# Performance work log

Hardware: AMD Instinct MI355X
Metric: run time of the kernel (lower is better)

Reference implementation:

```python
import jax, jax.numpy as jnp
import numpy as np

B, T, F, U = 128, 512, 512, 256

def hard_sigmoid(x):
    # Keras K.hard_sigmoid
    return jnp.clip(0.2 * x + 0.5, 0.0, 1.0)

def setup_inputs() -> dict:
    key = jax.random.key(0)
    ks = jax.random.split(key, 10)
    def glorot(k, shp):
        fan_in, fan_out = shp[0], shp[-1]
        std = np.sqrt(2.0 / (fan_in + fan_out)).astype(np.float32)
        return jax.random.normal(k, shp, jnp.float32) * std
    return {
        "x": jax.random.normal(ks[0], (B, T, F), jnp.float32),
        "kernel": glorot(ks[1], (F, 4 * U)),
        "recurrent_kernel": glorot(ks[2], (U, 4 * U)),
        "attention_h": glorot(ks[3], (F + U, U)),
        "attention_c": glorot(ks[4], (F + U, U)),
        "attention1": glorot(ks[5], (2 * U + F, U)),
        "biase1": glorot(ks[6], (U,)),
        "attention2": glorot(ks[7], (U, 1)),
        "attention2_2": glorot(ks[8], (U, 1)),
        "biase2": glorot(ks[9], (U,)),
    }

def _run_direction(x_tbf, xg_tbg, rk, Wh, Wc, units):
    # x_tbf: (T,B,F); xg_tbg: (T,B,4U) precomputed x @ kernel (same math as per-step dot)
    Bn = x_tbf.shape[1]
    z = jnp.zeros((Bn, units), x_tbf.dtype)
    carry0 = (z, z, z, z, z, z, z, z)

    def att_weights(states, Ws, xt):
        # softmax over L2 norms of tanh(concat(state, x) @ W) for 4 history states
        scores = []
        for s, W in zip(states, Ws):
            a = jnp.tanh(jnp.concatenate([s, xt], axis=1) @ W)  # (B,U)
            scores.append(jnp.sqrt(jnp.sum(a * a, axis=1)))     # (B,)
        return jax.nn.softmax(jnp.stack(scores, axis=1), axis=1)  # (B,4)

    def step(carry, inp):
        xt, xg = inp
        h1, c1, h2, c2, h3, c3, h4, c4 = carry
        wh = att_weights([h1, h2, h3, h4], [Wh, Wh, Wh, Wh], xt)
        hmix = jax.nn.relu(wh[:, 0:1] * h1 + wh[:, 1:2] * h2 + wh[:, 2:3] * h3 + wh[:, 3:4] * h4)
        # NOTE: original code (faithfully kept) uses attention_h for the 4th cell-state score
        wc = att_weights([c1, c2, c3, c4], [Wc, Wc, Wc, Wh], xt)
        cmix = jax.nn.relu(wc[:, 0:1] * c1 + wc[:, 1:2] * c2 + wc[:, 2:3] * c3 + wc[:, 3:4] * c4)
        g = xg + hmix @ rk  # (B,4U), gate order [i, f, c, o]
        i = hard_sigmoid(g[:, :units])
        f = hard_sigmoid(g[:, units:2 * units])
        m = hard_sigmoid(g[:, 2 * units:3 * units])  # candidate uses hard_sigmoid in original
        o = hard_sigmoid(g[:, 3 * units:])
        c = f * cmix + i * m
        h = o * jnp.tanh(c)
        # history shift: [h, c, h_tm1, c_tm1, h_tm2, c_tm2, h_tm3, c_tm3]
        return (h, c, h1, c1, h2, c2, h3, c3), h

    _, hs = jax.lax.scan(step, carry0, (x_tbf, xg_tbg))
    return hs  # (T,B,U)

def reference(x, kernel, recurrent_kernel, attention_h, attention_c,
              attention1, biase1, attention2, attention2_2, biase2):
    units = recurrent_kernel.shape[0]
    x_tbf = jnp.transpose(x, (1, 0, 2))              # (T,B,F)
    xg = jnp.einsum('tbf,fg->tbg', x_tbf, kernel)    # (T,B,4U)
    fwd = _run_direction(x_tbf, xg, recurrent_kernel, attention_h, attention_c, units)
    bwd = _run_direction(x_tbf[::-1], xg[::-1], recurrent_kernel, attention_h, attention_c, units)[::-1]
    outs = jnp.concatenate([fwd, bwd], axis=-1)      # (T,B,2U)
    outs = jnp.transpose(outs, (1, 0, 2))            # (B,T,2U)
    # intra attention (vectorized over time, equivalent to the per-step loop + reshape)
    A11 = attention1[:2 * units, :]
    A12 = attention1[2 * units:, :]
    ha = jax.nn.relu(outs @ A11 + 0.0 * biase1) @ attention2        # (B,T,1)
    hb = jax.nn.relu(x @ A12 + 0.0 * biase2) @ attention2_2         # (B,T,1)
    return jnp.tanh(ha * outs + hb)                                  # (B,T,2U)
```

## Files before the change

### kernel.cpp

```cpp
#include <hip/hip_runtime.h>
#include <cstddef>
#include <cstdint>

#define DEVINL __device__ __forceinline__

constexpr int Bn = 128;
constexpr int Tn = 512;
constexpr int Fn = 512;
constexpr int Un = 256;
constexpr int Gn = 1024;
constexpr int RS = 5;

typedef _Float16 h2t   __attribute__((ext_vector_type(2)));
typedef _Float16 half4 __attribute__((ext_vector_type(4)));
typedef _Float16 half8 __attribute__((ext_vector_type(8)));
typedef float    f32x4 __attribute__((ext_vector_type(4)));

DEVINL float ftanh(float x) { float e = __expf(2.f * x); return 1.f - 2.f / (e + 1.f); }
DEVINL float hsig(float x)  { return fminf(fmaxf(fmaf(x, 0.2f, 0.5f), 0.f), 1.f); }

DEVINL void softmax4(float* s) {
    float mx = fmaxf(fmaxf(s[0], s[1]), fmaxf(s[2], s[3]));
    float e0 = __expf(s[0] - mx), e1 = __expf(s[1] - mx);
    float e2 = __expf(s[2] - mx), e3 = __expf(s[3] - mx);
    float inv = 1.f / (e0 + e1 + e2 + e3);
    s[0] = e0 * inv; s[1] = e1 * inv; s[2] = e2 * inv; s[3] = e3 * inv;
}

DEVINL float d2(unsigned int w, unsigned int h, float acc) {
#if __has_builtin(__builtin_amdgcn_fdot2)
    return __builtin_amdgcn_fdot2(__builtin_bit_cast(h2t, w), __builtin_bit_cast(h2t, h), acc, false);
#else
    h2t a = __builtin_bit_cast(h2t, w), b = __builtin_bit_cast(h2t, h);
    acc = fmaf((float)a.x, (float)b.x, acc);
    acc = fmaf((float)a.y, (float)b.y, acc);
    return acc;
#endif
}
DEVINL float dot8h(uint4 w, uint4 h, float acc) {
    acc = d2(w.x, h.x, acc);
    acc = d2(w.y, h.y, acc);
    acc = d2(w.z, h.z, acc);
    acc = d2(w.w, h.w, acc);
    return acc;
}

__global__ __launch_bounds__(256)
void pack_x(const float* __restrict__ x, _Float16* __restrict__ xh)
{
    size_t i = ((size_t)blockIdx.x * 256 + threadIdx.x) * 4;
    float4 v = *(const float4*)(x + i);
    half4 o;
    o.x = (_Float16)v.x; o.y = (_Float16)v.y; o.z = (_Float16)v.z; o.w = (_Float16)v.w;
    *(half4*)(xh + i) = o;
}

__global__ __launch_bounds__(256)
void wt_pack(const float* __restrict__ W, _Float16* __restrict__ Wt, int N)
{
    int total = N * 512;
    for (int e = blockIdx.x * 256 + threadIdx.x; e < total; e += gridDim.x * 256) {
        int n = e >> 9, k = e & 511;
        Wt[e] = (_Float16)W[(size_t)k * N + n];
    }
}

__global__ __launch_bounds__(256)
void pack_w(const float* __restrict__ rk, const float* __restrict__ ath,
            const float* __restrict__ atc,
            _Float16* __restrict__ rkP, _Float16* __restrict__ WhP,
            _Float16* __restrict__ WcP)
{
    int idx = blockIdx.x * 256 + threadIdx.x;
    const int stride = gridDim.x * 256;
    for (int e = idx; e < 32 * 1024 * 8; e += stride) {
        int i = e & 7, n = (e >> 3) & 1023, kc = e >> 13;
        rkP[e] = (_Float16)rk[(size_t)(kc * 8 + i) * Gn + n];
    }
    for (int e = idx; e < 32 * 256 * 8; e += stride) {
        int i = e & 7, n = (e >> 3) & 255, kc = e >> 11;
        WhP[e] = (_Float16)ath[(size_t)(kc * 8 + i) * Un + n];
        WcP[e] = (_Float16)atc[(size_t)(kc * 8 + i) * Un + n];
    }
}

template<bool TMAJ>
__global__ __launch_bounds__(256)
void gemm_mfma(const _Float16* __restrict__ A, const _Float16* __restrict__ Wt,
               int N, _Float16* __restrict__ out)
{
    __shared__ __align__(16) _Float16 As[64][40];
    __shared__ __align__(16) _Float16 Bs[64][40];
    const int tid = threadIdx.x;
    const int n0 = blockIdx.x * 64, m0 = blockIdx.y * 64;
    const int w = tid >> 6, lane = tid & 63;
    const int fr = lane & 15, quad = lane >> 4;
    const int srow = tid >> 2, sk = (tid & 3) * 8;

    f32x4 acc[4];
    #pragma unroll
    for (int i = 0; i < 4; i++) acc[i] = (f32x4){0.f, 0.f, 0.f, 0.f};

    const _Float16* ap = A  + (size_t)(m0 + srow) * 512 + sk;
    const _Float16* bp = Wt + (size_t)(n0 + srow) * 512 + sk;

    for (int k0 = 0; k0 < 512; k0 += 32) {
        uint4 av = *(const uint4*)(ap + k0);
        uint4 bv = *(const uint4*)(bp + k0);
        __syncthreads();
        *(uint4*)&As[srow][sk] = av;
        *(uint4*)&Bs[srow][sk] = bv;
        __syncthreads();
        half8 a = *(const half8*)&As[w * 16 + fr][quad * 8];
        #pragma unroll
        for (int nt = 0; nt < 4; nt++) {
            half8 b = *(const half8*)&Bs[nt * 16 + fr][quad * 8];
            acc[nt] = __builtin_amdgcn_mfma_f32_16x16x32_f16(a, b, acc[nt], 0, 0, 0);
        }
    }
    #pragma unroll
    for (int nt = 0; nt < 4; nt++) {
        int n = n0 + nt * 16 + fr;
        #pragma unroll
        for (int reg = 0; reg < 4; reg++) {
            int m = m0 + w * 16 + quad * 4 + reg;
            if (TMAJ) {
                int b = m >> 9, t = m & 511;
                out[((size_t)t * Bn + b) * N + n] = (_Float16)acc[nt][reg];
            } else {
                out[(size_t)m * N + n] = (_Float16)acc[nt][reg];
            }
        }
    }
}

__global__ __launch_bounds__(512)
void recurrence(const _Float16* __restrict__ xg,
                const _Float16* __restrict__ xWh,
                const _Float16* __restrict__ xWc,
                const _Float16* __restrict__ rkP,
                const _Float16* __restrict__ WhP,
                const _Float16* __restrict__ WcP,
                _Float16* __restrict__ outs)
{
    const int tid = threadIdx.x;
    const int d = blockIdx.x >> 6;
    const int b0 = (blockIdx.x & 63) * 2;

    __shared__ float Hr[2][RS][Un], Cr[2][RS][Un];
    __shared__ float PHr[2][RS][Un], PCcr[2][RS][Un], PChr[2][RS][Un];
    __shared__ __align__(16) unsigned int hm_pk[2][128];
    __shared__ __align__(16) unsigned int Hpk[2][128], Cpk[2][128];
    __shared__ float gtmp[2][4][Un];
    __shared__ float red[2][8][4];
    __shared__ float wsm[2][8];

    for (int e = tid; e < 2 * RS * Un; e += 512) {
        ((float*)Hr)[e] = 0.f; ((float*)Cr)[e] = 0.f;
        ((float*)PHr)[e] = 0.f; ((float*)PCcr)[e] = 0.f; ((float*)PChr)[e] = 0.f;
    }
    __syncthreads();

    const int r = tid >> 8, u = tid & 255;
    const int lane = tid & 63, wv = tid >> 6;

    for (int t = 0; t < Tn; t++) {
        const int tt = d ? (Tn - 1 - t) : t;
        const int st = t % RS;
        int sj[4];
        #pragma unroll
        for (int j = 0; j < 4; j++) sj[j] = (t - 1 - j + 2 * RS) % RS;

        const size_t rowx = (size_t)tt * Bn + (b0 + r);

        float xh  = (float)xWh[rowx * Un + u];
        float xc  = (float)xWc[rowx * Un + u];
        float xg0 = (float)xg[rowx * Gn + u];
        float xg1 = (float)xg[rowx * Gn + Un + u];
        float xg2 = (float)xg[rowx * Gn + 2 * Un + u];
        float xg3 = (float)xg[rowx * Gn + 3 * Un + u];

        float vals[8];
        #pragma unroll
        for (int j = 0; j < 4; j++) {
            float ah = ftanh(PHr[r][sj[j]][u] + xh);
            vals[j] = ah * ah;
            float pc  = (j < 3) ? PCcr[r][sj[j]][u] : PChr[r][sj[j]][u];
            float ac = ftanh(pc + ((j < 3) ? xc : xh));
            vals[4 + j] = ac * ac;
        }
        #pragma unroll
        for (int jj = 0; jj < 8; jj++) {
            float v = vals[jj];
            #pragma unroll
            for (int m = 32; m; m >>= 1) v += __shfl_xor(v, m, 64);
            if (lane == 0) red[r][jj][wv & 3] = v;
        }
        __syncthreads();
        if (tid < 4) {
            int rr = tid >> 1, hf = tid & 1;
            float s[4];
            #pragma unroll
            for (int j = 0; j < 4; j++) {
                const float* q = red[rr][hf * 4 + j];
                s[j] = sqrtf(q[0] + q[1] + q[2] + q[3]);
            }
            softmax4(s);
            #pragma unroll
            for (int j = 0; j < 4; j++) wsm[rr][hf * 4 + j] = s[j];
        }
        __syncthreads();

        float ha = 0.f, ca = 0.f;
        #pragma unroll
        for (int j = 0; j < 4; j++) {
            ha = fmaf(wsm[r][j],     Hr[r][sj[j]][u], ha);
            ca = fmaf(wsm[r][4 + j], Cr[r][sj[j]][u], ca);
        }
        float hmv = fmaxf(ha, 0.f);
        float cmv = fmaxf(ca, 0.f);
        {
            float ho = __shfl_xor(hmv, 1, 64);
            if (!(tid & 1)) {
                h2t pk; pk.x = (_Float16)hmv; pk.y = (_Float16)ho;
                hm_pk[r][u >> 1] = __builtin_bit_cast(unsigned int, pk);
            }
        }
        __syncthreads();

        float a00 = 0.f, a01 = 0.f, a10 = 0.f, a11 = 0.f;
        {
            const _Float16* p1 = rkP + (size_t)tid * 8;
            const _Float16* p2 = rkP + (size_t)(tid + 512) * 8;
            #pragma unroll 4
            for (int kc = 0; kc < 32; kc++) {
                uint4 w1 = *(const uint4*)(p1 + (size_t)kc * 8192);
                uint4 w2 = *(const uint4*)(p2 + (size_t)kc * 8192);
                uint4 h0 = *(const uint4*)&hm_pk[0][kc * 4];
                uint4 h1 = *(const uint4*)&hm_pk[1][kc * 4];
                a00 = dot8h(w1, h0, a00); a01 = dot8h(w2, h0, a01);
                a10 = dot8h(w1, h1, a10); a11 = dot8h(w2, h1, a11);
            }
        }
        {
            int q1 = tid >> 8, u1 = tid & 255;
            gtmp[0][q1][u1] = a00;  gtmp[0][q1 + 2][u1] = a01;
            gtmp[1][q1][u1] = a10;  gtmp[1][q1 + 2][u1] = a11;
        }
        __syncthreads();

        {
            float g0 = gtmp[r][0][u] + xg0;
            float g1 = gtmp[r][1][u] + xg1;
            float g2 = gtmp[r][2][u] + xg2;
            float g3 = gtmp[r][3][u] + xg3;
            float gi = hsig(g0), gf = hsig(g1), gm = hsig(g2), go = hsig(g3);
            float c = gf * cmv + gi * gm;
            float h = go * ftanh(c);
            Hr[r][st][u] = h;
            Cr[r][st][u] = c;
            outs[(((size_t)(b0 + r)) * Tn + tt) * 512 + d * 256 + u] = (_Float16)h;
            float hho = __shfl_xor(h, 1, 64);
            float cco = __shfl_xor(c, 1, 64);
            if (!(tid & 1)) {
                h2t pk1; pk1.x = (_Float16)h; pk1.y = (_Float16)hho;
                h2t pk2; pk2.x = (_Float16)c; pk2.y = (_Float16)cco;
                Hpk[r][u >> 1] = __builtin_bit_cast(unsigned int, pk1);
                Cpk[r][u >> 1] = __builtin_bit_cast(unsigned int, pk2);
            }
        }
        __syncthreads();

        if (tid < 256) {
            const int c = tid;
            const _Float16* pw = WhP + (size_t)c * 8;
            float ph0 = 0.f, ph1 = 0.f, pc0 = 0.f, pc1 = 0.f;
            #pragma unroll 4
            for (int kc = 0; kc < 32; kc++) {
                uint4 wv4 = *(const uint4*)(pw + (size_t)kc * 2048);
                uint4 H0 = *(const uint4*)&Hpk[0][kc * 4];
                uint4 H1 = *(const uint4*)&Hpk[1][kc * 4];
                uint4 C0 = *(const uint4*)&Cpk[0][kc * 4];
                uint4 C1 = *(const uint4*)&Cpk[1][kc * 4];
                ph0 = dot8h(wv4, H0, ph0); ph1 = dot8h(wv4, H1, ph1);
                pc0 = dot8h(wv4, C0, pc0); pc1 = dot8h(wv4, C1, pc1);
            }
            PHr[0][st][c] = ph0; PHr[1][st][c] = ph1;
            PChr[0][st][c] = pc0; PChr[1][st][c] = pc1;
        } else {
            const int c = tid - 256;
            const _Float16* pw = WcP + (size_t)c * 8;
            float pc0 = 0.f, pc1 = 0.f;
            #pragma unroll 4
            for (int kc = 0; kc < 32; kc++) {
                uint4 wv4 = *(const uint4*)(pw + (size_t)kc * 2048);
                uint4 C0 = *(const uint4*)&Cpk[0][kc * 4];
                uint4 C1 = *(const uint4*)&Cpk[1][kc * 4];
                pc0 = dot8h(wv4, C0, pc0); pc1 = dot8h(wv4, C1, pc1);
            }
            PCcr[0][st][c] = pc0; PCcr[1][st][c] = pc1;
        }
        __syncthreads();
    }
}

DEVINL void cvt8(uint4 v, float* f) {
    h2t p0 = __builtin_bit_cast(h2t, v.x), p1 = __builtin_bit_cast(h2t, v.y);
    h2t p2 = __builtin_bit_cast(h2t, v.z), p3 = __builtin_bit_cast(h2t, v.w);
    f[0] = (float)p0.x; f[1] = (float)p0.y; f[2] = (float)p1.x; f[3] = (float)p1.y;
    f[4] = (float)p2.x; f[5] = (float)p2.y; f[6] = (float)p3.x; f[7] = (float)p3.y;
}

__global__ __launch_bounds__(256)
void final2(const _Float16* __restrict__ t1, const _Float16* __restrict__ t2,
            const _Float16* __restrict__ outs16,
            const float* __restrict__ at2, const float* __restrict__ at22,
            float* __restrict__ out)
{
    __shared__ float has[8], hbs[8];
    const int tid = threadIdx.x;
    const size_t m0 = (size_t)blockIdx.x * 8;
    const int rr = tid >> 5, us = tid & 31;
    const size_t m = m0 + rr;

    uint4 v1 = *(const uint4*)(t1 + m * 256 + us * 8);
    uint4 v2 = *(const uint4*)(t2 + m * 256 + us * 8);
    float f1[8], f2[8];
    cvt8(v1, f1); cvt8(v2, f2);
    float4 wa0 = *(const float4*)(at2  + us * 8);
    float4 wa1 = *(const float4*)(at2  + us * 8 + 4);
    float4 wb0 = *(const float4*)(at22 + us * 8);
    float4 wb1 = *(const float4*)(at22 + us * 8 + 4);

    float pa = fmaxf(f1[0], 0.f) * wa0.x + fmaxf(f1[1], 0.f) * wa0.y
             + fmaxf(f1[2], 0.f) * wa0.z + fmaxf(f1[3], 0.f) * wa0.w
             + fmaxf(f1[4], 0.f) * wa1.x + fmaxf(f1[5], 0.f) * wa1.y
             + fmaxf(f1[6], 0.f) * wa1.z + fmaxf(f1[7], 0.f) * wa1.w;
    float pb = fmaxf(f2[0], 0.f) * wb0.x + fmaxf(f2[1], 0.f) * wb0.y
             + fmaxf(f2[2], 0.f) * wb0.z + fmaxf(f2[3], 0.f) * wb0.w
             + fmaxf(f2[4], 0.f) * wb1.x + fmaxf(f2[5], 0.f) * wb1.y
             + fmaxf(f2[6], 0.f) * wb1.z + fmaxf(f2[7], 0.f) * wb1.w;
    #pragma unroll
    for (int mm = 16; mm; mm >>= 1) {
        pa += __shfl_xor(pa, mm, 32);
        pb += __shfl_xor(pb, mm, 32);
    }
    if (us == 0) { has[rr] = pa; hbs[rr] = pb; }
    __syncthreads();

    for (int e = tid; e < 8 * 128; e += 256) {
        int r2 = e >> 7, k4 = (e & 127) * 4;
        size_t base = (m0 + r2) * 512 + k4;
        uint2 hv = *(const uint2*)(outs16 + base);
        h2t pA = __builtin_bit_cast(h2t, hv.x), pB = __builtin_bit_cast(h2t, hv.y);
        float hav = has[r2], hbv = hbs[r2];
        float4 o;
        o.x = ftanh(hav * (float)pA.x + hbv);
        o.y = ftanh(hav * (float)pA.y + hbv);
        o.z = ftanh(hav * (float)pB.x + hbv);
        o.w = ftanh(hav * (float)pB.y + hbv);
        *(float4*)(out + base) = o;
    }
}

extern "C" void kernel_launch(void* const* d_in, const int* in_sizes, int n_in,
                              void* d_out, int out_size, void* d_ws, size_t ws_size,
                              hipStream_t stream)
{
    (void)in_sizes; (void)n_in; (void)out_size; (void)ws_size;
    const float* x    = (const float*)d_in[0];
    const float* wk   = (const float*)d_in[1];
    const float* rk   = (const float*)d_in[2];
    const float* ath  = (const float*)d_in[3];
    const float* atc  = (const float*)d_in[4];
    const float* at1  = (const float*)d_in[5];
    const float* at2  = (const float*)d_in[7];
    const float* at22 = (const float*)d_in[8];
    float* out = (float*)d_out;

    char* p = (char*)d_ws;
    auto take = [&](size_t bytes) { char* q = p; p += (bytes + 255) & ~(size_t)255; return q; };
    _Float16* xg   = (_Float16*)take((size_t)Tn * Bn * Gn * 2);
    _Float16* xWh  = (_Float16*)take((size_t)Tn * Bn * Un * 2);
    _Float16* xWc  = (_Float16*)take((size_t)Tn * Bn * Un * 2);
    _Float16* A16  = (_Float16*)take((size_t)Bn * Tn * 512 * 2);
    _Float16* xf16 = (_Float16*)take((size_t)Bn * Tn * Fn * 2);
    _Float16* rkP  = (_Float16*)take((size_t)Un * Gn * 2);
    _Float16* WhP  = (_Float16*)take((size_t)Un * Un * 2);
    _Float16* WcP  = (_Float16*)take((size_t)Un * Un * 2);
    _Float16* Wt1  = (_Float16*)take((size_t)Gn * Fn * 2);
    _Float16* Wt2  = (_Float16*)take((size_t)Un * Fn * 2);
    _Float16* Wt3  = (_Float16*)take((size_t)Un * Fn * 2);
    _Float16* WtA  = (_Float16*)take((size_t)Un * Fn * 2);
    _Float16* WtB  = (_Float16*)take((size_t)Un * Fn * 2);
    _Float16* t1 = (_Float16*)xg;
    _Float16* t2 = t1 + (size_t)Bn * Tn * Un;

    pack_x<<<32768, 256, 0, stream>>>(x, xf16);
    wt_pack<<<2048, 256, 0, stream>>>(wk, Wt1, Gn);
    wt_pack<<<1024, 256, 0, stream>>>(ath + (size_t)Un * Un, Wt2, Un);
    wt_pack<<<1024, 256, 0, stream>>>(atc + (size_t)Un * Un, Wt3, Un);
    wt_pack<<<1024, 256, 0, stream>>>(at1, WtA, Un);
    wt_pack<<<1024, 256, 0, stream>>>(at1 + (size_t)512 * Un, WtB, Un);
    pack_w<<<64, 256, 0, stream>>>(rk, ath, atc, rkP, WhP, WcP);

    gemm_mfma<true><<<dim3(Gn / 64, (Bn * Tn) / 64), 256, 0, stream>>>(xf16, Wt1, Gn, xg);
    gemm_mfma<true><<<dim3(Un / 64, (Bn * Tn) / 64), 256, 0, stream>>>(xf16, Wt2, Un, xWh);
    gemm_mfma<true><<<dim3(Un / 64, (Bn * Tn) / 64), 256, 0, stream>>>(xf16, Wt3, Un, xWc);

    recurrence<<<dim3(128), dim3(512), 0, stream>>>(xg, xWh, xWc, rkP, WhP, WcP, A16);

    gemm_mfma<false><<<dim3(Un / 64, (Bn * Tn) / 64), 256, 0, stream>>>(A16,  WtA, Un, t1);
    gemm_mfma<false><<<dim3(Un / 64, (Bn * Tn) / 64), 256, 0, stream>>>(xf16, WtB, Un, t2);
    final2<<<(Bn * Tn) / 8, 256, 0, stream>>>(t1, t2, A16, at2, at22, out);
}
```

Baseline: 5.469 ms.

## Double recurrence block to 1024 threads and fold softmax into all threads

```diff
diff --git a/kernel.cpp b/kernel.cpp
--- a/kernel.cpp
+++ b/kernel.cpp
@@ -134,7 +134,7 @@
     }
 }
 
-__global__ __launch_bounds__(512)
+__global__ __launch_bounds__(1024)
 void recurrence(const _Float16* __restrict__ xg,
                 const _Float16* __restrict__ xWh,
                 const _Float16* __restrict__ xWc,
@@ -152,17 +152,20 @@
     __shared__ __align__(16) unsigned int hm_pk[2][128];
     __shared__ __align__(16) unsigned int Hpk[2][128], Cpk[2][128];
     __shared__ float gtmp[2][4][Un];
-    __shared__ float red[2][8][4];
-    __shared__ float wsm[2][8];
-
-    for (int e = tid; e < 2 * RS * Un; e += 512) {
+    __shared__ __align__(16) float red[2][8][4];
+
+    for (int e = tid; e < 2 * RS * Un; e += 1024) {
         ((float*)Hr)[e] = 0.f; ((float*)Cr)[e] = 0.f;
         ((float*)PHr)[e] = 0.f; ((float*)PCcr)[e] = 0.f; ((float*)PChr)[e] = 0.f;
     }
     __syncthreads();
 
-    const int r = tid >> 8, u = tid & 255;
-    const int lane = tid & 63, wv = tid >> 6;
+    const int r2  = tid >> 9;
+    const int g   = (tid >> 8) & 1;
+    const int u   = tid & 255;
+    const int lane = tid & 63;
+    const int gwv = (tid >> 6) & 3;
+    const int r   = (tid >> 8) & 1;
 
     for (int t = 0; t < Tn; t++) {
         const int tt = d ? (Tn - 1 - t) : t;
@@ -171,55 +174,61 @@
         #pragma unroll
         for (int j = 0; j < 4; j++) sj[j] = (t - 1 - j + 2 * RS) % RS;
 
-        const size_t rowx = (size_t)tt * Bn + (b0 + r);
-
-        float xh  = (float)xWh[rowx * Un + u];
-        float xc  = (float)xWc[rowx * Un + u];
-        float xg0 = (float)xg[rowx * Gn + u];
-        float xg1 = (float)xg[rowx * Gn + Un + u];
-        float xg2 = (float)xg[rowx * Gn + 2 * Un + u];
-        float xg3 = (float)xg[rowx * Gn + 3 * Un + u];
-
-        float vals[8];
+        const size_t rowS = (size_t)tt * Bn + (b0 + r2);
+        float xh = (float)xWh[rowS * Un + u];
+        float xc = (float)xWc[rowS * Un + u];
+        float xg0 = 0.f, xg1 = 0.f, xg2 = 0.f, xg3 = 0.f;
+        if (tid < 512) {
+            const size_t rowG = (size_t)tt * Bn + (b0 + r);
+            xg0 = (float)xg[rowG * Gn + u];
+            xg1 = (float)xg[rowG * Gn + Un + u];
+            xg2 = (float)xg[rowG * Gn + 2 * Un + u];
+            xg3 = (float)xg[rowG * Gn + 3 * Un + u];
+        }
+
+        float vals[4];
+        if (g == 0) {
+            #pragma unroll
+            for (int j = 0; j < 4; j++) {
+                float ah = ftanh(PHr[r2][sj[j]][u] + xh);
+                vals[j] = ah * ah;
+            }
+        } else {
+            #pragma unroll
+            for (int j = 0; j < 4; j++) {
+                float pc = (j < 3) ? PCcr[r2][sj[j]][u] : PChr[r2][sj[j]][u];
+                float ac = ftanh(pc + ((j < 3) ? xc : xh));
+                vals[j] = ac * ac;
+            }
+        }
         #pragma unroll
-        for (int j = 0; j < 4; j++) {
-            float ah = ftanh(PHr[r][sj[j]][u] + xh);
-            vals[j] = ah * ah;
-            float pc  = (j < 3) ? PCcr[r][sj[j]][u] : PChr[r][sj[j]][u];
-            float ac = ftanh(pc + ((j < 3) ? xc : xh));
-            vals[4 + j] = ac * ac;
-        }
-        #pragma unroll
-        for (int jj = 0; jj < 8; jj++) {
+        for (int jj = 0; jj < 4; jj++) {
             float v = vals[jj];
             #pragma unroll
             for (int m = 32; m; m >>= 1) v += __shfl_xor(v, m, 64);
-            if (lane == 0) red[r][jj][wv & 3] = v;
-        }
-        __syncthreads();
-        if (tid < 4) {
-            int rr = tid >> 1, hf = tid & 1;
-            float s[4];
+            if (lane == 0) red[r2][g * 4 + jj][gwv] = v;
+        }
+        __syncthreads();
+
+        float cmv = 0.f;
+        if (tid < 512) {
+            float sh[4], sc[4];
             #pragma unroll
             for (int j = 0; j < 4; j++) {
-                const float* q = red[rr][hf * 4 + j];
-                s[j] = sqrtf(q[0] + q[1] + q[2] + q[3]);
-            }
-            softmax4(s);
+                float4 ph  = *(const float4*)red[r][j];
+                float4 pcv = *(const float4*)red[r][4 + j];
+                sh[j] = sqrtf(ph.x + ph.y + ph.z + ph.w);
+                sc[j] = sqrtf(pcv.x + pcv.y + pcv.z + pcv.w);
+            }
+            softmax4(sh); softmax4(sc);
+            float ha = 0.f, ca = 0.f;
             #pragma unroll
-            for (int j = 0; j < 4; j++) wsm[rr][hf * 4 + j] = s[j];
-        }
-        __syncthreads();
-
-        float ha = 0.f, ca = 0.f;
-        #pragma unroll
-        for (int j = 0; j < 4; j++) {
-            ha = fmaf(wsm[r][j],     Hr[r][sj[j]][u], ha);
-            ca = fmaf(wsm[r][4 + j], Cr[r][sj[j]][u], ca);
-        }
-        float hmv = fmaxf(ha, 0.f);
-        float cmv = fmaxf(ca, 0.f);
-        {
+            for (int j = 0; j < 4; j++) {
+                ha = fmaf(sh[j], Hr[r][sj[j]][u], ha);
+                ca = fmaf(sc[j], Cr[r][sj[j]][u], ca);
+            }
+            float hmv = fmaxf(ha, 0.f);
+            cmv = fmaxf(ca, 0.f);
             float ho = __shfl_xor(hmv, 1, 64);
             if (!(tid & 1)) {
                 h2t pk; pk.x = (_Float16)hmv; pk.y = (_Float16)ho;
@@ -228,28 +237,24 @@
         }
         __syncthreads();
 
-        float a00 = 0.f, a01 = 0.f, a10 = 0.f, a11 = 0.f;
         {
+            float a0 = 0.f, a1 = 0.f;
             const _Float16* p1 = rkP + (size_t)tid * 8;
-            const _Float16* p2 = rkP + (size_t)(tid + 512) * 8;
             #pragma unroll 4
             for (int kc = 0; kc < 32; kc++) {
                 uint4 w1 = *(const uint4*)(p1 + (size_t)kc * 8192);
-                uint4 w2 = *(const uint4*)(p2 + (size_t)kc * 8192);
                 uint4 h0 = *(const uint4*)&hm_pk[0][kc * 4];
                 uint4 h1 = *(const uint4*)&hm_pk[1][kc * 4];
-                a00 = dot8h(w1, h0, a00); a01 = dot8h(w2, h0, a01);
-                a10 = dot8h(w1, h1, a10); a11 = dot8h(w2, h1, a11);
-            }
-        }
-        {
-            int q1 = tid >> 8, u1 = tid & 255;
-            gtmp[0][q1][u1] = a00;  gtmp[0][q1 + 2][u1] = a01;
-            gtmp[1][q1][u1] = a10;  gtmp[1][q1 + 2][u1] = a11;
-        }
-        __syncthreads();
-
-        {
+                a0 = dot8h(w1, h0, a0);
+                a1 = dot8h(w1, h1, a1);
+            }
+            int q = tid >> 8, un = tid & 255;
+            gtmp[0][q][un] = a0;
+            gtmp[1][q][un] = a1;
+        }
+        __syncthreads();
+
+        if (tid < 512) {
             float g0 = gtmp[r][0][u] + xg0;
             float g1 = gtmp[r][1][u] + xg1;
             float g2 = gtmp[r][2][u] + xg2;
@@ -271,34 +276,32 @@
         }
         __syncthreads();
 
-        if (tid < 256) {
-            const int c = tid;
+        if (tid < 512) {
+            const int c = tid >> 1, rr = tid & 1;
             const _Float16* pw = WhP + (size_t)c * 8;
-            float ph0 = 0.f, ph1 = 0.f, pc0 = 0.f, pc1 = 0.f;
+            float ph = 0.f, pch = 0.f;
             #pragma unroll 4
             for (int kc = 0; kc < 32; kc++) {
                 uint4 wv4 = *(const uint4*)(pw + (size_t)kc * 2048);
-                uint4 H0 = *(const uint4*)&Hpk[0][kc * 4];
-                uint4 H1 = *(const uint4*)&Hpk[1][kc * 4];
-                uint4 C0 = *(const uint4*)&Cpk[0][kc * 4];
-                uint4 C1 = *(const uint4*)&Cpk[1][kc * 4];
-                ph0 = dot8h(wv4, H0, ph0); ph1 = dot8h(wv4, H1, ph1);
-                pc0 = dot8h(wv4, C0, pc0); pc1 = dot8h(wv4, C1, pc1);
-            }
-            PHr[0][st][c] = ph0; PHr[1][st][c] = ph1;
-            PChr[0][st][c] = pc0; PChr[1][st][c] = pc1;
+                uint4 Hv = *(const uint4*)&Hpk[rr][kc * 4];
+                uint4 Cv = *(const uint4*)&Cpk[rr][kc * 4];
+                ph  = dot8h(wv4, Hv, ph);
+                pch = dot8h(wv4, Cv, pch);
+            }
+            PHr[rr][st][c]  = ph;
+            PChr[rr][st][c] = pch;
         } else {
-            const int c = tid - 256;
+            const int i = tid - 512;
+            const int c = i >> 1, rr = i & 1;
             const _Float16* pw = WcP + (size_t)c * 8;
-            float pc0 = 0.f, pc1 = 0.f;
+            float pcc = 0.f;
             #pragma unroll 4
             for (int kc = 0; kc < 32; kc++) {
                 uint4 wv4 = *(const uint4*)(pw + (size_t)kc * 2048);
-                uint4 C0 = *(const uint4*)&Cpk[0][kc * 4];
-                uint4 C1 = *(const uint4*)&Cpk[1][kc * 4];
-                pc0 = dot8h(wv4, C0, pc0); pc1 = dot8h(wv4, C1, pc1);
-            }
-            PCcr[0][st][c] = pc0; PCcr[1][st][c] = pc1;
+                uint4 Cv = *(const uint4*)&Cpk[rr][kc * 4];
+                pcc = dot8h(wv4, Cv, pcc);
+            }
+            PCcr[rr][st][c] = pcc;
         }
         __syncthreads();
     }
@@ -408,7 +411,7 @@
     gemm_mfma<true><<<dim3(Un / 64, (Bn * Tn) / 64), 256, 0, stream>>>(xf16, Wt2, Un, xWh);
     gemm_mfma<true><<<dim3(Un / 64, (Bn * Tn) / 64), 256, 0, stream>>>(xf16, Wt3, Un, xWc);
 
-    recurrence<<<dim3(128), dim3(512), 0, stream>>>(xg, xWh, xWc, rkP, WhP, WcP, A16);
+    recurrence<<<dim3(128), dim3(1024), 0, stream>>>(xg, xWh, xWc, rkP, WhP, WcP, A16);
 
     gemm_mfma<false><<<dim3(Un / 64, (Bn * Tn) / 64), 256, 0, stream>>>(A16,  WtA, Un, t1);
     gemm_mfma<false><<<dim3(Un / 64, (Bn * Tn) / 64), 256, 0, stream>>>(xf16, WtB, Un, t2);
```

Measured after the change: 6.046 ms. 10.5% more time.
